# Performance work log

Measured on AMD Instinct MI355X. Metric: run time of the kernel, lower is better.

Reference implementation:

```python
import jax, jax.numpy as jnp
import numpy as np

NUM_HEADS = 16
WINDOW = 64


def setup_inputs() -> dict:
    key = jax.random.key(0)
    ks = jax.random.split(key, 6)
    b, l, d = 2, 2048, 1024
    s = 1.0 / np.sqrt(d)
    return {
        "x": jax.random.normal(ks[0], (b, l, d), dtype=jnp.float32),
        "Wq": jax.random.normal(ks[1], (d, d), dtype=jnp.float32) * s,
        "Wk": jax.random.normal(ks[2], (d, d), dtype=jnp.float32) * s,
        "Wv": jax.random.normal(ks[3], (d, d), dtype=jnp.float32) * s,
        "Wo": jax.random.normal(ks[4], (d, d), dtype=jnp.float32) * s,
        "bo": jax.random.normal(ks[5], (d,), dtype=jnp.float32) * 0.01,
    }


def reference(x, Wq, Wk, Wv, Wo, bo):
    b, l, d = x.shape
    h, w = NUM_HEADS, WINDOW
    dh = d // h
    p = w // 2
    # Projections. Padding is zeros and proj_k/proj_v have no bias, so
    # padding-then-projecting equals projecting-then-zero-padding.
    q = (x @ Wq.T).reshape(b, l, h, dh)                     # (b,l,h,dh)
    xp = jnp.pad(x, ((0, 0), (p, p), (0, 0)))               # (b,l+2p,d)
    k = (xp @ Wk.T).reshape(b, l + 2 * p, h, dh)
    v = (xp @ Wv.T).reshape(b, l + 2 * p, h, dh)
    # Sliding windows: query i attends to padded positions i .. i+w-1
    win_idx = jnp.arange(l)[:, None] + jnp.arange(w)[None, :]  # (l,w)
    kw = k[:, win_idx]                                       # (b,l,w,h,dh)
    vw = v[:, win_idx]                                       # (b,l,w,h,dh)
    scale = 1.0 / np.float32(np.sqrt(dh))
    scores = jnp.einsum('blhd,blwhd->blhw', q, kw) * scale   # (b,l,h,w)
    attn = jax.nn.softmax(scores, axis=-1)
    out = jnp.einsum('blhw,blwhd->blhd', attn, vw).reshape(b, l, d)
    return out @ Wo.T + bo
```

## Files before the change

### kernel.cpp

```cpp
#include <hip/hip_runtime.h>
#include <hip/hip_bf16.h>
#include <cstdint>

typedef __bf16 bf16;
typedef __bf16 bf16x4 __attribute__((ext_vector_type(4)));
typedef __bf16 bf16x8 __attribute__((ext_vector_type(8)));
typedef float floatx4 __attribute__((ext_vector_type(4)));

typedef __attribute__((address_space(1))) void as1_void;
typedef __attribute__((address_space(3))) void as3_void;

__device__ __forceinline__ void gld16(const void* g, void* l) {
#if __has_builtin(__builtin_amdgcn_global_load_lds)
  __builtin_amdgcn_global_load_lds((as1_void*)(uintptr_t)g, (as3_void*)l, 16, 0, 0);
#else
  *(uint4*)l = *(const uint4*)g;
#endif
}

__global__ __launch_bounds__(256) void convert_kernel(
    const float* __restrict__ x, const float* __restrict__ wq,
    const float* __restrict__ wk, const float* __restrict__ wv,
    const float* __restrict__ wo, bf16* __restrict__ xbf,
    bf16* __restrict__ wqkv, bf16* __restrict__ wob) {
  int i = blockIdx.x * 256 + threadIdx.x;
  const float* src;
  bf16* dst;
  int off;
  if (i < 1048576) {
    src = x; dst = xbf; off = i;
  } else if (i < 1310720) {
    src = wq; dst = wqkv; off = i - 1048576;
  } else if (i < 1572864) {
    src = wk; dst = wqkv + 1048576; off = i - 1310720;
  } else if (i < 1835008) {
    src = wv; dst = wqkv + 2097152; off = i - 1572864;
  } else {
    src = wo; dst = wob; off = i - 1835008;
  }
  float4 v = ((const float4*)src)[off];
  bf16x4 o;
  o[0] = (bf16)v.x; o[1] = (bf16)v.y; o[2] = (bf16)v.z; o[3] = (bf16)v.w;
  ((bf16x4*)dst)[off] = o;
}

template <int MODE>
__global__ __launch_bounds__(256) void gemm_nt(const bf16* __restrict__ A,
                                               const bf16* __restrict__ Bm,
                                               bf16* __restrict__ Cb,
                                               float* __restrict__ Cf,
                                               const float* __restrict__ bias,
                                               int M, int N, int K) {
  __shared__ __attribute__((aligned(16))) bf16 As[128 * 32];
  __shared__ __attribute__((aligned(16))) bf16 Bs[128 * 32];
  const int tid = threadIdx.x;
  const int lane = tid & 63;
  const int wave = tid >> 6;
  const int quad = lane >> 4;
  const int n0 = lane & 15;
  const int wm = wave >> 1;
  const int wn = wave & 1;
  const int bN = blockIdx.x, bM = blockIdx.y;
  const bf16* Ab = A + (size_t)bM * 128 * K;
  const bf16* Bb = Bm + (size_t)bN * 128 * K;
  const int c0 = tid, c1 = tid + 256;
  const int r0 = c0 >> 2, g0 = c0 & 3;
  const int r1 = c1 >> 2, g1 = c1 & 3;
  floatx4 acc[4][4] = {};
  for (int k0 = 0; k0 < K; k0 += 32) {
    gld16(Ab + (size_t)r0 * K + k0 + g0 * 8, &As[c0 * 8]);
    gld16(Ab + (size_t)r1 * K + k0 + g1 * 8, &As[c1 * 8]);
    gld16(Bb + (size_t)r0 * K + k0 + g0 * 8, &Bs[c0 * 8]);
    gld16(Bb + (size_t)r1 * K + k0 + g1 * 8, &Bs[c1 * 8]);
    __syncthreads();
    bf16x8 af[4], bfr[4];
#pragma unroll
    for (int mi = 0; mi < 4; ++mi)
      af[mi] = *(const bf16x8*)&As[(wm * 64 + mi * 16 + n0) * 32 + quad * 8];
#pragma unroll
    for (int ni = 0; ni < 4; ++ni)
      bfr[ni] = *(const bf16x8*)&Bs[(wn * 64 + ni * 16 + n0) * 32 + quad * 8];
#pragma unroll
    for (int mi = 0; mi < 4; ++mi)
#pragma unroll
      for (int ni = 0; ni < 4; ++ni)
        acc[mi][ni] = __builtin_amdgcn_mfma_f32_16x16x32_bf16(
            af[mi], bfr[ni], acc[mi][ni], 0, 0, 0);
    __syncthreads();
  }
  const int rowBase = bM * 128 + wm * 64;
  const int colBase = bN * 128 + wn * 64;
#pragma unroll
  for (int ni = 0; ni < 4; ++ni) {
    const int col = colBase + ni * 16 + n0;
    float badd = 0.f;
    if (MODE == 1) badd = bias[col];
#pragma unroll
    for (int mi = 0; mi < 4; ++mi)
#pragma unroll
      for (int r = 0; r < 4; ++r) {
        const int row = rowBase + mi * 16 + quad * 4 + r;
        if (MODE == 0)
          Cb[(size_t)row * N + col] = (bf16)acc[mi][ni][r];
        else
          Cf[(size_t)row * N + col] = acc[mi][ni][r] + badd;
      }
  }
}

__global__ __launch_bounds__(256) void attn_kernel(const bf16* __restrict__ qkv,
                                                   bf16* __restrict__ aout) {
  __shared__ __attribute__((aligned(16))) bf16 Qs[64 * 64];
  __shared__ __attribute__((aligned(16))) bf16 Ks[128 * 64];
  __shared__ __attribute__((aligned(16))) bf16 Vs[128 * 64];
  __shared__ __attribute__((aligned(16))) bf16 Ps[4 * 16 * 128];
  const int bid = blockIdx.x;
  const int b = bid >> 9;
  const int h = (bid >> 5) & 15;
  const int i0 = (bid & 31) * 64;
  const int tid = threadIdx.x;
  const int wave = tid >> 6, lane = tid & 63;
  const int quad = lane >> 4, n0 = lane & 15;

  for (int idx = tid; idx < 512; idx += 256) {
    const int r = idx >> 3, c = idx & 7;
    *(uint4*)&Qs[r * 64 + c * 8] =
        *(const uint4*)(qkv + (size_t)(b * 2048 + i0 + r) * 3072 + h * 64 + c * 8);
  }
  for (int idx = tid; idx < 2048; idx += 256) {
    const int kv = idx >> 10;
    const int r = (idx >> 3) & 127, c = idx & 7;
    const int j = i0 - 32 + r;
    uint4 val = make_uint4(0u, 0u, 0u, 0u);
    if (j >= 0 && j < 2048)
      val = *(const uint4*)(qkv + (size_t)(b * 2048 + j) * 3072 + 1024 +
                            kv * 1024 + h * 64 + c * 8);
    bf16* dst = kv ? Vs : Ks;
    *(uint4*)&dst[r * 64 + c * 8] = val;
  }
  __syncthreads();

  bf16x8 aq[2];
#pragma unroll
  for (int ks = 0; ks < 2; ++ks)
    aq[ks] = *(const bf16x8*)&Qs[(wave * 16 + n0) * 64 + ks * 32 + quad * 8];
  floatx4 accS[8] = {};
#pragma unroll
  for (int nt = 0; nt < 8; ++nt)
#pragma unroll
    for (int ks = 0; ks < 2; ++ks) {
      bf16x8 bk = *(const bf16x8*)&Ks[(nt * 16 + n0) * 64 + ks * 32 + quad * 8];
      accS[nt] = __builtin_amdgcn_mfma_f32_16x16x32_bf16(aq[ks], bk, accS[nt], 0, 0, 0);
    }

  float mrow[4] = {-1e30f, -1e30f, -1e30f, -1e30f};
#pragma unroll
  for (int nt = 0; nt < 8; ++nt)
#pragma unroll
    for (int r = 0; r < 4; ++r) {
      const int q64 = wave * 16 + quad * 4 + r;
      const int t = nt * 16 + n0;
      float s = accS[nt][r] * 0.125f;
      if (t < q64 || t >= q64 + 64) s = -1e30f;
      accS[nt][r] = s;
      mrow[r] = fmaxf(mrow[r], s);
    }
#pragma unroll
  for (int off = 1; off < 16; off <<= 1)
#pragma unroll
    for (int r = 0; r < 4; ++r)
      mrow[r] = fmaxf(mrow[r], __shfl_xor(mrow[r], off));
  float lrow[4] = {0.f, 0.f, 0.f, 0.f};
#pragma unroll
  for (int nt = 0; nt < 8; ++nt)
#pragma unroll
    for (int r = 0; r < 4; ++r) {
      const float e = __expf(accS[nt][r] - mrow[r]);
      accS[nt][r] = e;
      lrow[r] += e;
    }
#pragma unroll
  for (int off = 1; off < 16; off <<= 1)
#pragma unroll
    for (int r = 0; r < 4; ++r) lrow[r] += __shfl_xor(lrow[r], off);

  bf16* Pw = &Ps[wave * 2048];
#pragma unroll
  for (int r = 0; r < 4; ++r) {
    const float inv = 1.f / lrow[r];
#pragma unroll
    for (int nt = 0; nt < 8; ++nt)
      Pw[(quad * 4 + r) * 128 + nt * 16 + n0] = (bf16)(accS[nt][r] * inv);
  }

  floatx4 accO[4] = {};
#pragma unroll
  for (int kt = 0; kt < 4; ++kt) {
    bf16x8 ap = *(const bf16x8*)&Pw[n0 * 128 + kt * 32 + quad * 8];
#pragma unroll
    for (int dt = 0; dt < 4; ++dt) {
      bf16x8 bv;
#pragma unroll
      for (int jj = 0; jj < 8; ++jj)
        bv[jj] = Vs[(kt * 32 + quad * 8 + jj) * 64 + dt * 16 + n0];
      accO[dt] = __builtin_amdgcn_mfma_f32_16x16x32_bf16(ap, bv, accO[dt], 0, 0, 0);
    }
  }
#pragma unroll
  for (int dt = 0; dt < 4; ++dt)
#pragma unroll
    for (int r = 0; r < 4; ++r) {
      const int q64 = wave * 16 + quad * 4 + r;
      aout[(size_t)(b * 2048 + i0 + q64) * 1024 + h * 64 + dt * 16 + n0] =
          (bf16)accO[dt][r];
    }
}

extern "C" void kernel_launch(void* const* d_in, const int* in_sizes, int n_in,
                              void* d_out, int out_size, void* d_ws, size_t ws_size,
                              hipStream_t stream) {
  const float* x = (const float*)d_in[0];
  const float* wq = (const float*)d_in[1];
  const float* wk = (const float*)d_in[2];
  const float* wv = (const float*)d_in[3];
  const float* wo = (const float*)d_in[4];
  const float* bo = (const float*)d_in[5];
  char* ws = (char*)d_ws;
  bf16* xbf = (bf16*)(ws);
  bf16* wqkv = (bf16*)(ws + (8u << 20));
  bf16* wob = (bf16*)(ws + (14u << 20));
  bf16* qkv = (bf16*)(ws + (16u << 20));
  bf16* aout = xbf;

  convert_kernel<<<8192, 256, 0, stream>>>(x, wq, wk, wv, wo, xbf, wqkv, wob);
  gemm_nt<0><<<dim3(24, 32), 256, 0, stream>>>(xbf, wqkv, qkv, nullptr, nullptr,
                                               4096, 3072, 1024);
  attn_kernel<<<1024, 256, 0, stream>>>(qkv, aout);
  gemm_nt<1><<<dim3(8, 32), 256, 0, stream>>>(aout, wob, nullptr, (float*)d_out,
                                              bo, 4096, 1024, 1024);
}
```

Before: 170.9 us.

## Transpose V in shared memory, pad attention LDS, and narrow output GEMM tile

The attention kernel now pads K/V rows to avoid LDS bank conflicts, transposes V into a separate padded buffer so the PV MFMA operand is one 16-byte vector load instead of eight scalar loads, reads Q straight from global memory, and reuses the V buffer for P. The output-projection GEMM is templated on tile width and launched with 64-wide N tiles, giving 512 blocks instead of 256 to fill more compute units. The cost is an extra transpose pass with scalar LDS stores and an extra barrier in attention, plus lower per-block reuse in the narrower GEMM.

```diff
diff --git a/kernel.cpp b/kernel.cpp
--- a/kernel.cpp
+++ b/kernel.cpp
@@ -44,15 +44,17 @@
   ((bf16x4*)dst)[off] = o;
 }
 
-template <int MODE>
+template <int MODE, int BN>
 __global__ __launch_bounds__(256) void gemm_nt(const bf16* __restrict__ A,
                                                const bf16* __restrict__ Bm,
                                                bf16* __restrict__ Cb,
                                                float* __restrict__ Cf,
                                                const float* __restrict__ bias,
                                                int M, int N, int K) {
+  constexpr int WN = BN / 2;
+  constexpr int NI = WN / 16;
   __shared__ __attribute__((aligned(16))) bf16 As[128 * 32];
-  __shared__ __attribute__((aligned(16))) bf16 Bs[128 * 32];
+  __shared__ __attribute__((aligned(16))) bf16 Bs[BN * 32];
   const int tid = threadIdx.x;
   const int lane = tid & 63;
   const int wave = tid >> 6;
@@ -62,36 +64,37 @@
   const int wn = wave & 1;
   const int bN = blockIdx.x, bM = blockIdx.y;
   const bf16* Ab = A + (size_t)bM * 128 * K;
-  const bf16* Bb = Bm + (size_t)bN * 128 * K;
+  const bf16* Bb = Bm + (size_t)bN * BN * K;
   const int c0 = tid, c1 = tid + 256;
-  const int r0 = c0 >> 2, g0 = c0 & 3;
-  const int r1 = c1 >> 2, g1 = c1 & 3;
-  floatx4 acc[4][4] = {};
+  floatx4 acc[4][NI] = {};
   for (int k0 = 0; k0 < K; k0 += 32) {
-    gld16(Ab + (size_t)r0 * K + k0 + g0 * 8, &As[c0 * 8]);
-    gld16(Ab + (size_t)r1 * K + k0 + g1 * 8, &As[c1 * 8]);
-    gld16(Bb + (size_t)r0 * K + k0 + g0 * 8, &Bs[c0 * 8]);
-    gld16(Bb + (size_t)r1 * K + k0 + g1 * 8, &Bs[c1 * 8]);
+    gld16(Ab + (size_t)(c0 >> 2) * K + k0 + (c0 & 3) * 8, &As[c0 * 8]);
+    gld16(Ab + (size_t)(c1 >> 2) * K + k0 + (c1 & 3) * 8, &As[c1 * 8]);
+#pragma unroll
+    for (int cc = 0; cc < BN * 4; cc += 256) {
+      const int c = cc + tid;
+      gld16(Bb + (size_t)(c >> 2) * K + k0 + (c & 3) * 8, &Bs[c * 8]);
+    }
     __syncthreads();
-    bf16x8 af[4], bfr[4];
+    bf16x8 af[4], bfr[NI];
 #pragma unroll
     for (int mi = 0; mi < 4; ++mi)
       af[mi] = *(const bf16x8*)&As[(wm * 64 + mi * 16 + n0) * 32 + quad * 8];
 #pragma unroll
-    for (int ni = 0; ni < 4; ++ni)
-      bfr[ni] = *(const bf16x8*)&Bs[(wn * 64 + ni * 16 + n0) * 32 + quad * 8];
+    for (int ni = 0; ni < NI; ++ni)
+      bfr[ni] = *(const bf16x8*)&Bs[(wn * WN + ni * 16 + n0) * 32 + quad * 8];
 #pragma unroll
     for (int mi = 0; mi < 4; ++mi)
 #pragma unroll
-      for (int ni = 0; ni < 4; ++ni)
+      for (int ni = 0; ni < NI; ++ni)
         acc[mi][ni] = __builtin_amdgcn_mfma_f32_16x16x32_bf16(
             af[mi], bfr[ni], acc[mi][ni], 0, 0, 0);
     __syncthreads();
   }
   const int rowBase = bM * 128 + wm * 64;
-  const int colBase = bN * 128 + wn * 64;
-#pragma unroll
-  for (int ni = 0; ni < 4; ++ni) {
+  const int colBase = bN * BN + wn * WN;
+#pragma unroll
+  for (int ni = 0; ni < NI; ++ni) {
     const int col = colBase + ni * 16 + n0;
     float badd = 0.f;
     if (MODE == 1) badd = bias[col];
@@ -110,10 +113,9 @@
 
 __global__ __launch_bounds__(256) void attn_kernel(const bf16* __restrict__ qkv,
                                                    bf16* __restrict__ aout) {
-  __shared__ __attribute__((aligned(16))) bf16 Qs[64 * 64];
-  __shared__ __attribute__((aligned(16))) bf16 Ks[128 * 64];
-  __shared__ __attribute__((aligned(16))) bf16 Vs[128 * 64];
-  __shared__ __attribute__((aligned(16))) bf16 Ps[4 * 16 * 128];
+  __shared__ __attribute__((aligned(16))) bf16 Ks[128 * 72];
+  __shared__ __attribute__((aligned(16))) bf16 VsPs[128 * 72];
+  __shared__ __attribute__((aligned(16))) bf16 Vt[64 * 136];
   const int bid = blockIdx.x;
   const int b = bid >> 9;
   const int h = (bid >> 5) & 15;
@@ -121,35 +123,47 @@
   const int tid = threadIdx.x;
   const int wave = tid >> 6, lane = tid & 63;
   const int quad = lane >> 4, n0 = lane & 15;
-
-  for (int idx = tid; idx < 512; idx += 256) {
+  bf16* Vs = VsPs;
+
+#pragma unroll
+  for (int it = 0; it < 4; ++it) {
+    const int idx = it * 256 + tid;
     const int r = idx >> 3, c = idx & 7;
-    *(uint4*)&Qs[r * 64 + c * 8] =
-        *(const uint4*)(qkv + (size_t)(b * 2048 + i0 + r) * 3072 + h * 64 + c * 8);
-  }
-  for (int idx = tid; idx < 2048; idx += 256) {
-    const int kv = idx >> 10;
-    const int r = (idx >> 3) & 127, c = idx & 7;
     const int j = i0 - 32 + r;
-    uint4 val = make_uint4(0u, 0u, 0u, 0u);
-    if (j >= 0 && j < 2048)
-      val = *(const uint4*)(qkv + (size_t)(b * 2048 + j) * 3072 + 1024 +
-                            kv * 1024 + h * 64 + c * 8);
-    bf16* dst = kv ? Vs : Ks;
-    *(uint4*)&dst[r * 64 + c * 8] = val;
+    uint4 kv_ = make_uint4(0u, 0u, 0u, 0u);
+    uint4 vv = make_uint4(0u, 0u, 0u, 0u);
+    if (j >= 0 && j < 2048) {
+      const bf16* base = qkv + (size_t)(b * 2048 + j) * 3072 + 1024 + h * 64 + c * 8;
+      kv_ = *(const uint4*)base;
+      vv = *(const uint4*)(base + 1024);
+    }
+    *(uint4*)&Ks[r * 72 + c * 8] = kv_;
+    *(uint4*)&Vs[r * 72 + c * 8] = vv;
   }
   __syncthreads();
 
+#pragma unroll
+  for (int it = 0; it < 4; ++it) {
+    const int idx = it * 256 + tid;
+    const int t = idx & 127, c = idx >> 7;
+    bf16x8 v = *(const bf16x8*)&Vs[t * 72 + c * 8];
+#pragma unroll
+    for (int jj = 0; jj < 8; ++jj) Vt[(c * 8 + jj) * 136 + t] = v[jj];
+  }
+  __syncthreads();
+
   bf16x8 aq[2];
 #pragma unroll
   for (int ks = 0; ks < 2; ++ks)
-    aq[ks] = *(const bf16x8*)&Qs[(wave * 16 + n0) * 64 + ks * 32 + quad * 8];
+    aq[ks] = *(const bf16x8*)(qkv +
+        (size_t)(b * 2048 + i0 + wave * 16 + n0) * 3072 + h * 64 + ks * 32 + quad * 8);
+
   floatx4 accS[8] = {};
 #pragma unroll
   for (int nt = 0; nt < 8; ++nt)
 #pragma unroll
     for (int ks = 0; ks < 2; ++ks) {
-      bf16x8 bk = *(const bf16x8*)&Ks[(nt * 16 + n0) * 64 + ks * 32 + quad * 8];
+      bf16x8 bk = *(const bf16x8*)&Ks[(nt * 16 + n0) * 72 + ks * 32 + quad * 8];
       accS[nt] = __builtin_amdgcn_mfma_f32_16x16x32_bf16(aq[ks], bk, accS[nt], 0, 0, 0);
     }
 
@@ -184,25 +198,22 @@
 #pragma unroll
     for (int r = 0; r < 4; ++r) lrow[r] += __shfl_xor(lrow[r], off);
 
-  bf16* Pw = &Ps[wave * 2048];
+  bf16* Pw = &VsPs[wave * 16 * 136];
 #pragma unroll
   for (int r = 0; r < 4; ++r) {
     const float inv = 1.f / lrow[r];
 #pragma unroll
     for (int nt = 0; nt < 8; ++nt)
-      Pw[(quad * 4 + r) * 128 + nt * 16 + n0] = (bf16)(accS[nt][r] * inv);
+      Pw[(quad * 4 + r) * 136 + nt * 16 + n0] = (bf16)(accS[nt][r] * inv);
   }
 
   floatx4 accO[4] = {};
 #pragma unroll
   for (int kt = 0; kt < 4; ++kt) {
-    bf16x8 ap = *(const bf16x8*)&Pw[n0 * 128 + kt * 32 + quad * 8];
+    bf16x8 ap = *(const bf16x8*)&Pw[n0 * 136 + kt * 32 + quad * 8];
 #pragma unroll
     for (int dt = 0; dt < 4; ++dt) {
-      bf16x8 bv;
-#pragma unroll
-      for (int jj = 0; jj < 8; ++jj)
-        bv[jj] = Vs[(kt * 32 + quad * 8 + jj) * 64 + dt * 16 + n0];
+      bf16x8 bv = *(const bf16x8*)&Vt[(dt * 16 + n0) * 136 + kt * 32 + quad * 8];
       accO[dt] = __builtin_amdgcn_mfma_f32_16x16x32_bf16(ap, bv, accO[dt], 0, 0, 0);
     }
   }
@@ -233,9 +244,10 @@
   bf16* aout = xbf;
 
   convert_kernel<<<8192, 256, 0, stream>>>(x, wq, wk, wv, wo, xbf, wqkv, wob);
-  gemm_nt<0><<<dim3(24, 32), 256, 0, stream>>>(xbf, wqkv, qkv, nullptr, nullptr,
-                                               4096, 3072, 1024);
+  gemm_nt<0, 128><<<dim3(24, 32), 256, 0, stream>>>(xbf, wqkv, qkv, nullptr,
+                                                    nullptr, 4096, 3072, 1024);
   attn_kernel<<<1024, 256, 0, stream>>>(qkv, aout);
-  gemm_nt<1><<<dim3(8, 32), 256, 0, stream>>>(aout, wob, nullptr, (float*)d_out,
-                                              bo, 4096, 1024, 1024);
-}
+  gemm_nt<1, 64><<<dim3(16, 32), 256, 0, stream>>>(aout, wob, nullptr,
+                                                   (float*)d_out, bo, 4096, 1024,
+                                                   1024);
+}
```

After: 157.8 us. -7.7%, faster.
